# Kernel optimization log

Hardware: AMD Instinct MI355X
Metric: run time of the kernel (lower is better)

The kernel has to match this reference:

```python
import jax, jax.numpy as jnp
import numpy as np

DIM = 1024
HEADS = 16
HEAD_DIM = DIM // HEADS
B, S = 4, 2048


def setup_inputs() -> dict:
    key = jax.random.key(0)
    ks = jax.random.split(key, 12)
    scale = 1.0 / np.sqrt(DIM)
    inp = {
        "q": jax.random.normal(ks[0], (B, S, DIM), jnp.float32),
        "k": jax.random.normal(ks[1], (B, S, DIM), jnp.float32),
        "v": jax.random.normal(ks[2], (B, S, DIM), jnp.float32),
        "Wq": jax.random.normal(ks[3], (DIM, DIM), jnp.float32) * scale,
        "bq": jax.random.normal(ks[4], (DIM,), jnp.float32) * 0.01,
        "Wk": jax.random.normal(ks[5], (DIM, DIM), jnp.float32) * scale,
        "bk": jax.random.normal(ks[6], (DIM,), jnp.float32) * 0.01,
        "Wv": jax.random.normal(ks[7], (DIM, DIM), jnp.float32) * scale,
        "bv": jax.random.normal(ks[8], (DIM,), jnp.float32) * 0.01,
        "Wo": jax.random.normal(ks[9], (DIM, DIM), jnp.float32) * scale,
        "bo": jax.random.normal(ks[10], (DIM,), jnp.float32) * 0.01,
        "mask": jax.random.randint(ks[11], (B, S, S), 0, 2, jnp.int32),
    }
    return inp


def reference(q, k, v, Wq, bq, Wk, bk, Wv, bv, Wo, bo, mask):
    # QKV projections, split into heads: [B, H, S, Dh]
    def proj(x, W, b):
        y = x @ W + b
        return y.reshape(B, S, HEADS, HEAD_DIM).transpose(0, 2, 1, 3)

    qh, kh, vh = proj(q, Wq, bq), proj(k, Wk, bk), proj(v, Wv, bv)

    # scaled dot-product attention with additive mask fill (-1e9 where mask==0)
    score = jnp.einsum('bhqd,bhkd->bhqk', qh, kh) / jnp.sqrt(jnp.float32(HEAD_DIM))
    score = jnp.where(mask[:, None, :, :] == 0, jnp.float32(-1e9), score)
    attn = jax.nn.softmax(score, axis=-1)  # dropout p=0.0 -> identity

    out = jnp.einsum('bhqk,bhkd->bhqd', attn, vh)
    out = out.transpose(0, 2, 1, 3).reshape(B, S, DIM)
    return out @ Wo + bo
```

## Files before the change

kernel.cpp:

```cpp
#include <hip/hip_runtime.h>
#include <cstdint>
#include <cstddef>

#define BB 4
#define SS 2048
#define DIMM 1024
#define NH 16
#define DH 64
#define MT 8192

typedef __attribute__((ext_vector_type(8))) short bf16x8;
typedef __attribute__((ext_vector_type(4))) float f32x4;
typedef __attribute__((ext_vector_type(4))) unsigned short u16x4;
typedef __attribute__((ext_vector_type(4))) unsigned int uint32x4;

#define MFMA_BF16(a, b, c) __builtin_amdgcn_mfma_f32_16x16x32_bf16(a, b, c, 0, 0, 0)

#define QSCALE 0.1803368801111137f

__device__ __forceinline__ unsigned short f2b(float f) {
    unsigned int u = __float_as_uint(f);
    u += 0x7fffu + ((u >> 16) & 1u);
    return (unsigned short)(u >> 16);
}

__device__ __forceinline__ unsigned int cvtpk(float lo, float hi) {
    unsigned int r;
    asm("v_cvt_pk_bf16_f32 %0, %1, %2" : "=v"(r) : "v"(lo), "v"(hi));
    return r;
}

__device__ __forceinline__ float fexp2(float x) {
    float r;
    asm("v_exp_f32 %0, %1" : "=v"(r) : "v"(x));
    return r;
}

__device__ __forceinline__ void gload16(const void* g, void* l) {
    __builtin_amdgcn_global_load_lds(
        (const __attribute__((address_space(1))) unsigned int*)g,
        (__attribute__((address_space(3))) unsigned int*)l, 16, 0, 0);
}

__device__ __forceinline__ int swzb(int row, int cb) {
    return row * 128 + (((cb) ^ (row & 7)) << 4);
}

__global__ __launch_bounds__(256)
void maskpack_kernel(const int* __restrict__ m, unsigned long long* __restrict__ mp)
{
    const size_t i = (size_t)blockIdx.x * 256 + threadIdx.x;
    const unsigned long long bal = __ballot(m[i] != 0);
    if ((threadIdx.x & 63) == 0) mp[i >> 6] = bal;
}

__global__ __launch_bounds__(256)
void convert_kernel(const float* __restrict__ s0, const float* __restrict__ s1,
                    const float* __restrict__ s2, unsigned short* __restrict__ d0,
                    unsigned short* __restrict__ d1, unsigned short* __restrict__ d2)
{
    const float* src = (blockIdx.y == 0) ? s0 : (blockIdx.y == 1) ? s1 : s2;
    unsigned short* dst = (blockIdx.y == 0) ? d0 : (blockIdx.y == 1) ? d1 : d2;
    const size_t i = ((size_t)blockIdx.x * 256 + threadIdx.x) * 8;
    const float4 lo = *reinterpret_cast<const float4*>(src + i);
    const float4 hi = *reinterpret_cast<const float4*>(src + i + 4);
    uint32x4 w = {cvtpk(lo.x, lo.y), cvtpk(lo.z, lo.w),
                  cvtpk(hi.x, hi.y), cvtpk(hi.z, hi.w)};
    *reinterpret_cast<uint32x4*>(dst + i) = w;
}

__global__ __launch_bounds__(256)
void wtrans_kernel(const float* __restrict__ W, unsigned short* __restrict__ WT, float scale)
{
    __shared__ unsigned short T[64][72];
    const int tid = threadIdx.x;
    const int k0 = blockIdx.y * 64, n0 = blockIdx.x * 64;
#pragma unroll
    for (int it = 0; it < 4; ++it) {
        const int c = tid + it * 256;
        const int row = c >> 4, c4 = (c & 15) * 4;
        const float4 v = *reinterpret_cast<const float4*>(&W[(size_t)(k0 + row) * DIMM + n0 + c4]);
        T[row][c4 + 0] = f2b(v.x * scale);
        T[row][c4 + 1] = f2b(v.y * scale);
        T[row][c4 + 2] = f2b(v.z * scale);
        T[row][c4 + 3] = f2b(v.w * scale);
    }
    __syncthreads();
#pragma unroll
    for (int it = 0; it < 4; ++it) {
        const int c = tid + it * 256;
        const int n = c >> 4, k4 = (c & 15) * 4;
        u16x4 o;
        o[0] = T[k4 + 0][n];
        o[1] = T[k4 + 1][n];
        o[2] = T[k4 + 2][n];
        o[3] = T[k4 + 3][n];
        *reinterpret_cast<u16x4*>(&WT[(size_t)(n0 + n) * DIMM + k0 + k4]) = o;
    }
}

__global__ __launch_bounds__(256)
void gemm_qkv_kernel(const unsigned short* __restrict__ Qb,
                     const unsigned short* __restrict__ Kb,
                     const unsigned short* __restrict__ Vb,
                     const unsigned short* __restrict__ WT3,
                     const float* __restrict__ bq, const float* __restrict__ bk,
                     const float* __restrict__ bv,
                     unsigned short* __restrict__ Qh, unsigned short* __restrict__ Kh,
                     unsigned short* __restrict__ VhT)
{
    __shared__ __align__(16) unsigned short As[128 * 32];
    __shared__ __align__(16) unsigned short Bs[128 * 32];
    const int tid = threadIdx.x;
    const int w = tid >> 6, l = tid & 63;
    const int g = l >> 4, li = l & 15;
    const int bid = blockIdx.x;
    const int swz = (bid & 7) * 192 + (bid >> 3);
    const int region = swz >> 9;
    const int rl = swz & 511;
    const int m0 = (rl >> 3) * 128, n0 = (rl & 7) * 128;
    const int wm0 = (w >> 1) * 64, wn0 = (w & 1) * 64;

    const unsigned short* A = (region == 0) ? Qb : (region == 1) ? Kb : Vb;
    const unsigned short* BT = WT3 + (size_t)region * (DIMM * DIMM);

    const f32x4 fzero = {0.f, 0.f, 0.f, 0.f};
    f32x4 acc[4][4];
#pragma unroll
    for (int i = 0; i < 4; ++i)
#pragma unroll
        for (int j = 0; j < 4; ++j) acc[i][j] = fzero;

    for (int k0 = 0; k0 < DIMM; k0 += 32) {
#pragma unroll
        for (int it = 0; it < 2; ++it) {
            const int c = it * 256 + w * 64 + l;
            const int row = c >> 2, cb = c & 3;
            gload16(&A[(size_t)(m0 + row) * DIMM + k0 + cb * 8],
                    &As[(it * 256 + w * 64) * 8]);
        }
#pragma unroll
        for (int it = 0; it < 2; ++it) {
            const int c = it * 256 + w * 64 + l;
            const int row = c >> 2, cb = c & 3;
            gload16(&BT[(size_t)(n0 + row) * DIMM + k0 + cb * 8],
                    &Bs[(it * 256 + w * 64) * 8]);
        }
        __syncthreads();

        bf16x8 af[4], bf[4];
#pragma unroll
        for (int mb = 0; mb < 4; ++mb)
            af[mb] = *reinterpret_cast<const bf16x8*>(&As[(wm0 + mb * 16 + li) * 32 + g * 8]);
#pragma unroll
        for (int nb = 0; nb < 4; ++nb)
            bf[nb] = *reinterpret_cast<const bf16x8*>(&Bs[(wn0 + nb * 16 + li) * 32 + g * 8]);
#pragma unroll
        for (int mb = 0; mb < 4; ++mb)
#pragma unroll
            for (int nb = 0; nb < 4; ++nb)
                acc[mb][nb] = MFMA_BF16(af[mb], bf[nb], acc[mb][nb]);
        __syncthreads();
    }

    const float* bias = (region == 0) ? bq : (region == 1) ? bk : bv;
    const float bscale = (region == 0) ? QSCALE : 1.0f;
    float bv4[4];
#pragma unroll
    for (int nb = 0; nb < 4; ++nb)
        bv4[nb] = bias[n0 + wn0 + nb * 16 + li] * bscale;

    unsigned short* dst = (region == 0) ? Qh : (region == 1) ? Kh : VhT;
#pragma unroll
    for (int mb = 0; mb < 4; ++mb) {
#pragma unroll
        for (int r = 0; r < 4; ++r) {
            const int row_g = m0 + wm0 + mb * 16 + g * 4 + r;
#pragma unroll
            for (int nb = 0; nb < 4; ++nb) {
                const int col = n0 + wn0 + nb * 16 + li;
                const float val = acc[mb][nb][r] + bv4[nb];
                const int bb = row_g >> 11, s = row_g & 2047;
                const int hh = col >> 6, dd = col & 63;
                if (region < 2) {
                    dst[(((size_t)(bb * NH + hh)) * SS + s) * DH + dd] = f2b(val);
                } else {
                    const int st = s & 63;
                    const int sp = (st & 32) + ((st >> 2) & 3) * 8 + ((st & 16) >> 2) + (st & 3);
                    dst[(((size_t)(bb * NH + hh)) * DH + dd) * SS + (s & ~63) + sp] = f2b(val);
                }
            }
        }
    }
}

__global__ __launch_bounds__(256)
void gemm_out_kernel(const unsigned short* __restrict__ Ax, const unsigned short* __restrict__ BT,
                     const float* __restrict__ bias, float* __restrict__ Y)
{
    __shared__ __align__(16) unsigned short As[128 * 32];
    __shared__ __align__(16) unsigned short Bs[128 * 32];
    const int tid = threadIdx.x;
    const int w = tid >> 6, l = tid & 63;
    const int g = l >> 4, li = l & 15;
    const int bid = blockIdx.x;
    const int swz = (bid & 7) * 64 + (bid >> 3);
    const int m0 = (swz >> 3) * 128, n0 = (swz & 7) * 128;
    const int wm0 = (w >> 1) * 64, wn0 = (w & 1) * 64;

    const f32x4 fzero = {0.f, 0.f, 0.f, 0.f};
    f32x4 acc[4][4];
#pragma unroll
    for (int i = 0; i < 4; ++i)
#pragma unroll
        for (int j = 0; j < 4; ++j) acc[i][j] = fzero;

    for (int k0 = 0; k0 < DIMM; k0 += 32) {
        const int h = k0 >> 6;
#pragma unroll
        for (int it = 0; it < 2; ++it) {
            const int c = it * 256 + w * 64 + l;
            const int row = c >> 2, cb = c & 3;
            const int m = m0 + row;
            const int bb = m >> 11, s = m & 2047;
            gload16(&Ax[(((size_t)(bb * NH + h)) * SS + s) * DH + (k0 & 63) + cb * 8],
                    &As[(it * 256 + w * 64) * 8]);
        }
#pragma unroll
        for (int it = 0; it < 2; ++it) {
            const int c = it * 256 + w * 64 + l;
            const int row = c >> 2, cb = c & 3;
            gload16(&BT[(size_t)(n0 + row) * DIMM + k0 + cb * 8],
                    &Bs[(it * 256 + w * 64) * 8]);
        }
        __syncthreads();

        bf16x8 af[4], bf[4];
#pragma unroll
        for (int mb = 0; mb < 4; ++mb)
            af[mb] = *reinterpret_cast<const bf16x8*>(&As[(wm0 + mb * 16 + li) * 32 + g * 8]);
#pragma unroll
        for (int nb = 0; nb < 4; ++nb)
            bf[nb] = *reinterpret_cast<const bf16x8*>(&Bs[(wn0 + nb * 16 + li) * 32 + g * 8]);
#pragma unroll
        for (int mb = 0; mb < 4; ++mb)
#pragma unroll
            for (int nb = 0; nb < 4; ++nb)
                acc[mb][nb] = MFMA_BF16(af[mb], bf[nb], acc[mb][nb]);
        __syncthreads();
    }

    float bv4[4];
#pragma unroll
    for (int nb = 0; nb < 4; ++nb)
        bv4[nb] = bias[n0 + wn0 + nb * 16 + li];

#pragma unroll
    for (int mb = 0; mb < 4; ++mb) {
#pragma unroll
        for (int r = 0; r < 4; ++r) {
            const int row_g = m0 + wm0 + mb * 16 + g * 4 + r;
#pragma unroll
            for (int nb = 0; nb < 4; ++nb) {
                const int col = n0 + wn0 + nb * 16 + li;
                Y[(size_t)row_g * DIMM + col] = acc[mb][nb][r] + bv4[nb];
            }
        }
    }
}

__global__ __launch_bounds__(256)
void flash_kernel(const unsigned short* __restrict__ Qh, const unsigned short* __restrict__ Kh,
                  const unsigned short* __restrict__ VhT, const unsigned long long* __restrict__ maskp,
                  unsigned short* __restrict__ Ctx)
{
    const int qt = blockIdx.x, h = blockIdx.y, b = blockIdx.z;
    const int tid = threadIdx.x;
    const int w = tid >> 6, l = tid & 63;
    const int g = l >> 4, li = l & 15;

    __shared__ __align__(16) unsigned short smem[4 * 64 * 64];
    __shared__ unsigned int LUT4[4];

    const int q0 = qt * 128;
    const size_t hb = ((size_t)(b * NH + h)) * (size_t)(SS * DH);

    if (tid < 4) LUT4[tid] = ((tid & 1) ? 0xFFFFu : 0u) | ((tid & 2) ? 0xFFFF0000u : 0u);

    bf16x8 qf[2][2];
#pragma unroll
    for (int qc = 0; qc < 2; ++qc) {
        const unsigned short* qp = &Qh[hb + (size_t)(q0 + w * 32 + qc * 16 + li) * DH + g * 8];
        qf[qc][0] = *reinterpret_cast<const bf16x8*>(qp);
        qf[qc][1] = *reinterpret_cast<const bf16x8*>(qp + 32);
    }

    bf16x8 vones;
#pragma unroll
    for (int j = 0; j < 8; ++j) vones[j] = (short)0x3F80;

    const f32x4 fzero = {0.f, 0.f, 0.f, 0.f};
    f32x4 oacc[2][4];
    f32x4 lacc[2];
#pragma unroll
    for (int qc = 0; qc < 2; ++qc) {
        lacc[qc] = fzero;
#pragma unroll
        for (int mb = 0; mb < 4; ++mb) oacc[qc][mb] = fzero;
    }

    int ks_[2], vs_[2];
#pragma unroll
    for (int it = 0; it < 2; ++it) {
        const int c = it * 256 + w * 64 + l;
        const int row = c >> 3, cb = (c & 7) ^ (row & 7);
        ks_[it] = row * DH + cb * 8;
        vs_[it] = row * SS + cb * 8;
    }
    const unsigned short* Ksrc = Kh + hb;
    const unsigned short* Vsrc = VhT + hb;
    const unsigned long long* mrow_p = maskp + ((size_t)(b * SS + q0 + w * 32 + li)) * 32;

#define STAGE(bn, tt) do {                                                      \
    gload16(Ksrc + (size_t)(tt) * 4096 + ks_[0], smem + (bn) * 4096 + w * 512); \
    gload16(Ksrc + (size_t)(tt) * 4096 + ks_[1], smem + (bn) * 4096 + 2048 + w * 512); \
    gload16(Vsrc + (size_t)(tt) * 64 + vs_[0], smem + 8192 + (bn) * 4096 + w * 512);   \
    gload16(Vsrc + (size_t)(tt) * 64 + vs_[1], smem + 8192 + (bn) * 4096 + 2048 + w * 512); \
} while (0)

    STAGE(0, 0);
    __syncthreads();

    int buf = 0;
    for (int t = 0; t < SS / 64; ++t) {
        if (t < SS / 64 - 1) STAGE(buf ^ 1, t + 1);

        const unsigned long long mw0 = mrow_p[t];
        const unsigned long long mw1 = mrow_p[512 + t];

        const char* Kc = (const char*)(smem + buf * 4096);
        bf16x8 kf[4][2];
#pragma unroll
        for (int nb = 0; nb < 4; ++nb)
#pragma unroll
            for (int hh = 0; hh < 2; ++hh)
                kf[nb][hh] = *reinterpret_cast<const bf16x8*>(
                    Kc + (nb * 16 + li) * 128 + (((hh * 4 + g) ^ (li & 7)) << 4));

        bf16x8 pf[2][2];
#pragma unroll
        for (int qc = 0; qc < 2; ++qc) {
            f32x4 st[4];
#pragma unroll
            for (int nb = 0; nb < 4; ++nb) st[nb] = fzero;
            __builtin_amdgcn_s_setprio(1);
#pragma unroll
            for (int nb = 0; nb < 4; ++nb)
#pragma unroll
                for (int hh = 0; hh < 2; ++hh)
                    st[nb] = MFMA_BF16(kf[nb][hh], qf[qc][hh], st[nb]);
            __builtin_amdgcn_s_setprio(0);

            float e[4][4];
#pragma unroll
            for (int nb = 0; nb < 4; ++nb)
#pragma unroll
                for (int r = 0; r < 4; ++r)
                    e[nb][r] = fexp2(st[nb][r]);

            const unsigned long long msh = (qc ? mw1 : mw0) >> (g * 4);
            const unsigned lo = (unsigned)msh, hi = (unsigned)(msh >> 32);
            uint32x4 w0 = {cvtpk(e[0][0], e[0][1]), cvtpk(e[0][2], e[0][3]),
                           cvtpk(e[1][0], e[1][1]), cvtpk(e[1][2], e[1][3])};
            uint32x4 w1 = {cvtpk(e[2][0], e[2][1]), cvtpk(e[2][2], e[2][3]),
                           cvtpk(e[3][0], e[3][1]), cvtpk(e[3][2], e[3][3])};
            w0[0] &= LUT4[lo & 3u];         w0[1] &= LUT4[(lo >> 2) & 3u];
            w0[2] &= LUT4[(lo >> 16) & 3u]; w0[3] &= LUT4[(lo >> 18) & 3u];
            w1[0] &= LUT4[hi & 3u];         w1[1] &= LUT4[(hi >> 2) & 3u];
            w1[2] &= LUT4[(hi >> 16) & 3u]; w1[3] &= LUT4[(hi >> 18) & 3u];
            pf[qc][0] = __builtin_bit_cast(bf16x8, w0);
            pf[qc][1] = __builtin_bit_cast(bf16x8, w1);
        }

        const char* Vc = (const char*)(smem + 8192 + buf * 4096);
        bf16x8 vf[4][2];
#pragma unroll
        for (int mb = 0; mb < 4; ++mb)
#pragma unroll
            for (int hh = 0; hh < 2; ++hh)
                vf[mb][hh] = *reinterpret_cast<const bf16x8*>(
                    Vc + (mb * 16 + li) * 128 + (((hh * 4 + g) ^ (li & 7)) << 4));

#pragma unroll
        for (int qc = 0; qc < 2; ++qc) {
            __builtin_amdgcn_s_setprio(1);
#pragma unroll
            for (int hh = 0; hh < 2; ++hh)
#pragma unroll
                for (int mb = 0; mb < 4; ++mb)
                    oacc[qc][mb] = MFMA_BF16(pf[qc][hh], vf[mb][hh], oacc[qc][mb]);
            lacc[qc] = MFMA_BF16(pf[qc][0], vones, lacc[qc]);
            lacc[qc] = MFMA_BF16(pf[qc][1], vones, lacc[qc]);
            __builtin_amdgcn_s_setprio(0);
        }

        __syncthreads();
        buf ^= 1;
    }
#undef STAGE

    unsigned short* Ps = smem;
#pragma unroll
    for (int qc = 0; qc < 2; ++qc) {
#pragma unroll
        for (int r = 0; r < 4; ++r) {
            const int row = w * 32 + qc * 16 + g * 4 + r;
            const float linv = 1.0f / lacc[qc][r];
#pragma unroll
            for (int mb = 0; mb < 4; ++mb) {
                const int dd = mb * 16 + li;
                *(unsigned short*)((char*)Ps + swzb(row, dd >> 3) + (dd & 7) * 2) =
                    f2b(oacc[qc][mb][r] * linv);
            }
        }
    }
    __syncthreads();
#pragma unroll
    for (int it = 0; it < 4; ++it) {
        const int c = it * 64 + l;
        const int qrow = w * 32 + (c >> 3), cb = c & 7;
        const bf16x8 ov = *reinterpret_cast<const bf16x8*>((const char*)Ps + swzb(qrow, cb));
        *reinterpret_cast<bf16x8*>(&Ctx[hb + (size_t)(q0 + qrow) * DH + cb * 8]) = ov;
    }
}

extern "C" void kernel_launch(void* const* d_in, const int* in_sizes, int n_in,
                              void* d_out, int out_size, void* d_ws, size_t ws_size,
                              hipStream_t stream)
{
    const float* q  = (const float*)d_in[0];
    const float* k  = (const float*)d_in[1];
    const float* v  = (const float*)d_in[2];
    const float* Wq = (const float*)d_in[3];
    const float* bq = (const float*)d_in[4];
    const float* Wk = (const float*)d_in[5];
    const float* bk = (const float*)d_in[6];
    const float* Wv = (const float*)d_in[7];
    const float* bv = (const float*)d_in[8];
    const float* Wo = (const float*)d_in[9];
    const float* bo = (const float*)d_in[10];
    const int* mask = (const int*)d_in[11];
    float* out = (float*)d_out;

    const size_t M1 = 1048576, M8 = (size_t)MT * DIMM;
    unsigned short* WT3 = (unsigned short*)d_ws;
    unsigned short* WTo = WT3 + 3 * M1;
    unsigned short* Qb  = WTo + M1;
    unsigned short* Kb  = Qb + M8;
    unsigned short* Vb  = Kb + M8;
    unsigned short* Qh  = Vb + M8;
    unsigned short* Kh  = Qh + M8;
    unsigned long long* maskp = (unsigned long long*)(Kh + M8);
    unsigned short* VhT = (unsigned short*)(maskp + (size_t)BB * SS * SS / 64);
    unsigned short* Ctx = Kb;

    dim3 blk(256);

    maskpack_kernel<<<dim3((unsigned)((size_t)BB * SS * SS / 256)), blk, 0, stream>>>(mask, maskp);

    dim3 tgrid(16, 16);
    wtrans_kernel<<<tgrid, blk, 0, stream>>>(Wq, WT3, QSCALE);
    wtrans_kernel<<<tgrid, blk, 0, stream>>>(Wk, WT3 + M1, 1.0f);
    wtrans_kernel<<<tgrid, blk, 0, stream>>>(Wv, WT3 + 2 * M1, 1.0f);
    wtrans_kernel<<<tgrid, blk, 0, stream>>>(Wo, WTo, 1.0f);

    convert_kernel<<<dim3(4096, 3), blk, 0, stream>>>(q, k, v, Qb, Kb, Vb);

    gemm_qkv_kernel<<<dim3(1536), blk, 0, stream>>>(Qb, Kb, Vb, WT3, bq, bk, bv,
                                                    Qh, Kh, VhT);

    dim3 fgrid(SS / 128, NH, BB);
    flash_kernel<<<fgrid, blk, 0, stream>>>(Qh, Kh, VhT, maskp, Ctx);

    gemm_out_kernel<<<dim3(512), blk, 0, stream>>>(Ctx, WTo, bo, out);
}
```

Measured before the change: 305.7 us.

## Fuse prep kernels into one launch, reorder flash grid, tweak swizzle and occupancy

Merges the mask packing, the fp32→bf16 input conversion and the four weight-transpose launches into a single prep kernel that dispatches on block index, removing five kernel launches and their tail gaps. It also swaps the software bf16 rounding for the hardware packed-convert instruction, changes the QKV GEMM block swizzle so each region is contiguous, reorders the flash grid so heads are the fastest-varying index, and adds a min-blocks-per-CU hint of 4 to the flash kernel. The occupancy hint may force register spilling, and the grid reorders change L2 locality in ways that are hard to predict.

```diff
diff --git a/kernel.cpp b/kernel.cpp
--- a/kernel.cpp
+++ b/kernel.cpp
@@ -18,18 +18,16 @@
 
 #define QSCALE 0.1803368801111137f
 
-__device__ __forceinline__ unsigned short f2b(float f) {
-    unsigned int u = __float_as_uint(f);
-    u += 0x7fffu + ((u >> 16) & 1u);
-    return (unsigned short)(u >> 16);
-}
-
 __device__ __forceinline__ unsigned int cvtpk(float lo, float hi) {
     unsigned int r;
     asm("v_cvt_pk_bf16_f32 %0, %1, %2" : "=v"(r) : "v"(lo), "v"(hi));
     return r;
 }
 
+__device__ __forceinline__ unsigned short f2b1(float f) {
+    return (unsigned short)cvtpk(f, f);
+}
+
 __device__ __forceinline__ float fexp2(float x) {
     float r;
     asm("v_exp_f32 %0, %1" : "=v"(r) : "v"(x));
@@ -47,55 +45,64 @@
 }
 
 __global__ __launch_bounds__(256)
-void maskpack_kernel(const int* __restrict__ m, unsigned long long* __restrict__ mp)
-{
-    const size_t i = (size_t)blockIdx.x * 256 + threadIdx.x;
-    const unsigned long long bal = __ballot(m[i] != 0);
-    if ((threadIdx.x & 63) == 0) mp[i >> 6] = bal;
-}
-
-__global__ __launch_bounds__(256)
-void convert_kernel(const float* __restrict__ s0, const float* __restrict__ s1,
-                    const float* __restrict__ s2, unsigned short* __restrict__ d0,
-                    unsigned short* __restrict__ d1, unsigned short* __restrict__ d2)
-{
-    const float* src = (blockIdx.y == 0) ? s0 : (blockIdx.y == 1) ? s1 : s2;
-    unsigned short* dst = (blockIdx.y == 0) ? d0 : (blockIdx.y == 1) ? d1 : d2;
-    const size_t i = ((size_t)blockIdx.x * 256 + threadIdx.x) * 8;
-    const float4 lo = *reinterpret_cast<const float4*>(src + i);
-    const float4 hi = *reinterpret_cast<const float4*>(src + i + 4);
-    uint32x4 w = {cvtpk(lo.x, lo.y), cvtpk(lo.z, lo.w),
-                  cvtpk(hi.x, hi.y), cvtpk(hi.z, hi.w)};
-    *reinterpret_cast<uint32x4*>(dst + i) = w;
-}
-
-__global__ __launch_bounds__(256)
-void wtrans_kernel(const float* __restrict__ W, unsigned short* __restrict__ WT, float scale)
+void prep_kernel(const float* __restrict__ q, const float* __restrict__ k,
+                 const float* __restrict__ v,
+                 unsigned short* __restrict__ Qb, unsigned short* __restrict__ Kb,
+                 unsigned short* __restrict__ Vb,
+                 const int* __restrict__ mask, unsigned long long* __restrict__ mp,
+                 const float* __restrict__ Wq, const float* __restrict__ Wk,
+                 const float* __restrict__ Wv, const float* __restrict__ Wo,
+                 unsigned short* __restrict__ WT3, unsigned short* __restrict__ WTo)
 {
     __shared__ unsigned short T[64][72];
     const int tid = threadIdx.x;
-    const int k0 = blockIdx.y * 64, n0 = blockIdx.x * 64;
-#pragma unroll
-    for (int it = 0; it < 4; ++it) {
-        const int c = tid + it * 256;
-        const int row = c >> 4, c4 = (c & 15) * 4;
-        const float4 v = *reinterpret_cast<const float4*>(&W[(size_t)(k0 + row) * DIMM + n0 + c4]);
-        T[row][c4 + 0] = f2b(v.x * scale);
-        T[row][c4 + 1] = f2b(v.y * scale);
-        T[row][c4 + 2] = f2b(v.z * scale);
-        T[row][c4 + 3] = f2b(v.w * scale);
-    }
-    __syncthreads();
-#pragma unroll
-    for (int it = 0; it < 4; ++it) {
-        const int c = tid + it * 256;
-        const int n = c >> 4, k4 = (c & 15) * 4;
-        u16x4 o;
-        o[0] = T[k4 + 0][n];
-        o[1] = T[k4 + 1][n];
-        o[2] = T[k4 + 2][n];
-        o[3] = T[k4 + 3][n];
-        *reinterpret_cast<u16x4*>(&WT[(size_t)(n0 + n) * DIMM + k0 + k4]) = o;
+    const int bid = blockIdx.x;
+
+    if (bid < 12288) {
+        const int which = bid >> 12;
+        const float* src = (which == 0) ? q : (which == 1) ? k : v;
+        unsigned short* dst = (which == 0) ? Qb : (which == 1) ? Kb : Vb;
+        const size_t i = ((size_t)(bid & 4095) * 256 + tid) * 8;
+        const float4 lo = *reinterpret_cast<const float4*>(src + i);
+        const float4 hi = *reinterpret_cast<const float4*>(src + i + 4);
+        uint32x4 w = {cvtpk(lo.x, lo.y), cvtpk(lo.z, lo.w),
+                      cvtpk(hi.x, hi.y), cvtpk(hi.z, hi.w)};
+        *reinterpret_cast<uint32x4*>(dst + i) = w;
+    } else if (bid < 77824) {
+        const size_t i = (size_t)(bid - 12288) * 256 + tid;
+        const unsigned long long bal = __ballot(mask[i] != 0);
+        if ((tid & 63) == 0) mp[i >> 6] = bal;
+    } else {
+        const int wb = bid - 77824;
+        const int which = wb >> 8;
+        const float* W = (which == 0) ? Wq : (which == 1) ? Wk : (which == 2) ? Wv : Wo;
+        unsigned short* WT = (which < 3) ? (WT3 + (size_t)which * DIMM * DIMM) : WTo;
+        const float scale = (which == 0) ? QSCALE : 1.0f;
+        const int within = wb & 255;
+        const int n0 = (within & 15) * 64, k0 = (within >> 4) * 64;
+#pragma unroll
+        for (int it = 0; it < 4; ++it) {
+            const int c = tid + it * 256;
+            const int row = c >> 4, c4 = (c & 15) * 4;
+            const float4 vv = *reinterpret_cast<const float4*>(
+                &W[(size_t)(k0 + row) * DIMM + n0 + c4]);
+            T[row][c4 + 0] = f2b1(vv.x * scale);
+            T[row][c4 + 1] = f2b1(vv.y * scale);
+            T[row][c4 + 2] = f2b1(vv.z * scale);
+            T[row][c4 + 3] = f2b1(vv.w * scale);
+        }
+        __syncthreads();
+#pragma unroll
+        for (int it = 0; it < 4; ++it) {
+            const int c = tid + it * 256;
+            const int n = c >> 4, k4 = (c & 15) * 4;
+            u16x4 o;
+            o[0] = T[k4 + 0][n];
+            o[1] = T[k4 + 1][n];
+            o[2] = T[k4 + 2][n];
+            o[3] = T[k4 + 3][n];
+            *reinterpret_cast<u16x4*>(&WT[(size_t)(n0 + n) * DIMM + k0 + k4]) = o;
+        }
     }
 }
 
@@ -115,10 +122,10 @@
     const int w = tid >> 6, l = tid & 63;
     const int g = l >> 4, li = l & 15;
     const int bid = blockIdx.x;
-    const int swz = (bid & 7) * 192 + (bid >> 3);
-    const int region = swz >> 9;
-    const int rl = swz & 511;
-    const int m0 = (rl >> 3) * 128, n0 = (rl & 7) * 128;
+    const int region = bid >> 9;
+    const int rl = bid & 511;
+    const int swz = (rl & 7) * 64 + (rl >> 3);
+    const int m0 = (swz >> 3) * 128, n0 = (swz & 7) * 128;
     const int wm0 = (w >> 1) * 64, wn0 = (w & 1) * 64;
 
     const unsigned short* A = (region == 0) ? Qb : (region == 1) ? Kb : Vb;
@@ -183,11 +190,11 @@
                 const int bb = row_g >> 11, s = row_g & 2047;
                 const int hh = col >> 6, dd = col & 63;
                 if (region < 2) {
-                    dst[(((size_t)(bb * NH + hh)) * SS + s) * DH + dd] = f2b(val);
+                    dst[(((size_t)(bb * NH + hh)) * SS + s) * DH + dd] = f2b1(val);
                 } else {
                     const int st = s & 63;
                     const int sp = (st & 32) + ((st >> 2) & 3) * 8 + ((st & 16) >> 2) + (st & 3);
-                    dst[(((size_t)(bb * NH + hh)) * DH + dd) * SS + (s & ~63) + sp] = f2b(val);
+                    dst[(((size_t)(bb * NH + hh)) * DH + dd) * SS + (s & ~63) + sp] = f2b1(val);
                 }
             }
         }
@@ -269,12 +276,12 @@
     }
 }
 
-__global__ __launch_bounds__(256)
+__global__ __launch_bounds__(256, 4)
 void flash_kernel(const unsigned short* __restrict__ Qh, const unsigned short* __restrict__ Kh,
                   const unsigned short* __restrict__ VhT, const unsigned long long* __restrict__ maskp,
                   unsigned short* __restrict__ Ctx)
 {
-    const int qt = blockIdx.x, h = blockIdx.y, b = blockIdx.z;
+    const int h = blockIdx.x, qt = blockIdx.y, b = blockIdx.z;
     const int tid = threadIdx.x;
     const int w = tid >> 6, l = tid & 63;
     const int g = l >> 4, li = l & 15;
@@ -420,7 +427,7 @@
             for (int mb = 0; mb < 4; ++mb) {
                 const int dd = mb * 16 + li;
                 *(unsigned short*)((char*)Ps + swzb(row, dd >> 3) + (dd & 7) * 2) =
-                    f2b(oacc[qc][mb][r] * linv);
+                    f2b1(oacc[qc][mb][r] * linv);
             }
         }
     }
@@ -466,20 +473,14 @@
 
     dim3 blk(256);
 
-    maskpack_kernel<<<dim3((unsigned)((size_t)BB * SS * SS / 256)), blk, 0, stream>>>(mask, maskp);
-
-    dim3 tgrid(16, 16);
-    wtrans_kernel<<<tgrid, blk, 0, stream>>>(Wq, WT3, QSCALE);
-    wtrans_kernel<<<tgrid, blk, 0, stream>>>(Wk, WT3 + M1, 1.0f);
-    wtrans_kernel<<<tgrid, blk, 0, stream>>>(Wv, WT3 + 2 * M1, 1.0f);
-    wtrans_kernel<<<tgrid, blk, 0, stream>>>(Wo, WTo, 1.0f);
-
-    convert_kernel<<<dim3(4096, 3), blk, 0, stream>>>(q, k, v, Qb, Kb, Vb);
+    prep_kernel<<<dim3(78848), blk, 0, stream>>>(q, k, v, Qb, Kb, Vb,
+                                                 mask, maskp,
+                                                 Wq, Wk, Wv, Wo, WT3, WTo);
 
     gemm_qkv_kernel<<<dim3(1536), blk, 0, stream>>>(Qb, Kb, Vb, WT3, bq, bk, bv,
                                                     Qh, Kh, VhT);
 
-    dim3 fgrid(SS / 128, NH, BB);
+    dim3 fgrid(NH, SS / 128, BB);
     flash_kernel<<<fgrid, blk, 0, stream>>>(Qh, Kh, VhT, maskp, Ctx);
 
     gemm_out_kernel<<<dim3(512), blk, 0, stream>>>(Ctx, WTo, bo, out);
```

Result: faster. 274.7 us (-10.1%).
